# Kernel tuning notes

Hardware: AMD Instinct MI355X
Metric: run time of the kernel (lower is better)

Reference implementation:

```python
import jax, jax.numpy as jnp
import numpy as np

B, N, C = 8, 4096, 64          # graphs, points per graph, feature dim
RATIO = 0.25
M = int(N * RATIO)             # 1024 sampled centroids per graph
R = 0.2                        # radius (points live in the unit cube)
K = 64                         # max_num_neighbors in the forward
BIG = 1e10


def fps_single(pos):
    """Farthest point sampling on one cloud. pos: [N,3] -> [M] local indices.
    Deterministic start at index 0 (PyG uses a random start; math is identical)."""
    n = pos.shape[0]

    def step(carry, _):
        mind, last = carry
        d = jnp.sum((pos - pos[last]) ** 2, axis=-1)      # [N]
        mind = jnp.minimum(mind, d)
        nxt = jnp.argmax(mind)
        return (mind, nxt), nxt

    init = (jnp.full((n,), BIG, pos.dtype), jnp.int32(0))
    _, rest = jax.lax.scan(step, init, None, length=M - 1)
    return jnp.concatenate([jnp.zeros((1,), rest.dtype), rest])


def setup_inputs() -> dict:
    key = jax.random.key(0)
    ks = jax.random.split(key, 8)
    x = jax.random.normal(ks[0], (B * N, C), dtype=jnp.float32)
    pos = jax.random.uniform(ks[1], (B * N, 3), dtype=jnp.float32)
    batch = jnp.repeat(jnp.arange(B, dtype=jnp.int64), N)
    seed_idx = jnp.arange(B * N, dtype=jnp.int64)
    d_in, h, f_out = C + 3, 128, 256
    W1 = jax.random.normal(ks[2], (d_in, h), dtype=jnp.float32) / np.sqrt(d_in)
    b1 = jnp.zeros((h,), jnp.float32)
    W2 = jax.random.normal(ks[3], (h, h), dtype=jnp.float32) / np.sqrt(h)
    b2 = jnp.zeros((h,), jnp.float32)
    W3 = jax.random.normal(ks[4], (h, f_out), dtype=jnp.float32) / np.sqrt(h)
    b3 = jnp.zeros((f_out,), jnp.float32)
    return {"x": x, "pos": pos, "batch": batch, "seed_idx": seed_idx,
            "W1": W1, "b1": b1, "W2": W2, "b2": b2, "W3": W3, "b3": b3}


def reference(x, pos, batch, seed_idx, W1, b1, W2, b2, W3, b3):
    posb = pos.reshape(B, N, 3)
    xb = x.reshape(B, N, C)

    # --- FPS per graph (batch is block-contiguous with N points per graph) ---
    idx_local = jax.vmap(fps_single)(posb)                     # [B, M]
    ctr = jax.vmap(lambda p, i: p[i])(posb, idx_local)         # [B, M, 3]

    # --- radius neighbor search: up to K neighbors within r of each centroid ---
    d2 = jnp.sum((ctr[:, :, None, :] - posb[:, None, :, :]) ** 2, axis=-1)  # [B,M,N]
    d2m = jnp.where(d2 < R * R, d2, BIG)
    neg_d, nbr = jax.lax.top_k(-d2m, K)                        # K nearest within r
    valid = (-neg_d) < R * R                                   # [B, M, K]

    # --- PointConv: msg = MLP([x_j, pos_j - pos_i]), max-aggregate ---
    x_j = jax.vmap(lambda a, i: a[i])(xb, nbr)                 # [B, M, K, C]
    pos_j = jax.vmap(lambda p, i: p[i])(posb, nbr)             # [B, M, K, 3]
    msg = jnp.concatenate([x_j, pos_j - ctr[:, :, None, :]], axis=-1)  # [B,M,K,C+3]
    h = jax.nn.relu(msg @ W1 + b1)
    h = jax.nn.relu(h @ W2 + b2)
    h = jax.nn.relu(h @ W3 + b3)                               # [B, M, K, 256]
    h = jnp.where(valid[..., None], h, -BIG)
    out = jnp.max(h, axis=2)                                   # [B, M, 256]
    out = jnp.where(jnp.any(valid, axis=-1)[..., None], out, 0.0)

    # --- gather sampled outputs back to the flat layout ---
    idx_flat = (idx_local + jnp.arange(B)[:, None] * N).reshape(-1)  # [B*M]
    x_out = out.reshape(B * M, -1)
    pos_out = pos[idx_flat]
    batch_out = batch[idx_flat]
    seed_out = seed_idx[idx_flat]
    return x_out, pos_out, batch_out, seed_out
```

## Files before the change

kernel.cpp:

```cpp
#include <hip/hip_runtime.h>
#include <stdint.h>

#define BB 8
#define NN 4096
#define CC 64
#define MM 1024
#define EE (BB*MM)
#define KK 64
#define F3 256
#define SM 104
#define SH 136
#define CAP 768

typedef __bf16 bf16x8 __attribute__((ext_vector_type(8)));
typedef float floatx4 __attribute__((ext_vector_type(4)));

#define DPP_MAXSTEP(ctrl, rmask) { \
    unsigned o = (unsigned)__builtin_amdgcn_update_dpp(0, (int)v, ctrl, rmask, 0xf, false); \
    v = v > o ? v : o; }
__device__ __forceinline__ unsigned wave_umax_u32(unsigned v) {
  DPP_MAXSTEP(0x111, 0xf)
  DPP_MAXSTEP(0x112, 0xf)
  DPP_MAXSTEP(0x114, 0xf)
  DPP_MAXSTEP(0x118, 0xf)
  DPP_MAXSTEP(0x142, 0xa)
  DPP_MAXSTEP(0x143, 0xc)
  return (unsigned)__builtin_amdgcn_readlane((int)v, 63);
}
#define DPP_MINSTEP(ctrl, rmask) { \
    unsigned o = (unsigned)__builtin_amdgcn_update_dpp((int)0xffffffffu, (int)v, ctrl, rmask, 0xf, false); \
    v = v < o ? v : o; }
__device__ __forceinline__ unsigned wave_umin_u32(unsigned v) {
  DPP_MINSTEP(0x111, 0xf)
  DPP_MINSTEP(0x112, 0xf)
  DPP_MINSTEP(0x114, 0xf)
  DPP_MINSTEP(0x118, 0xf)
  DPP_MINSTEP(0x142, 0xa)
  DPP_MINSTEP(0x143, 0xc)
  return (unsigned)__builtin_amdgcn_readlane((int)v, 63);
}


__global__ __launch_bounds__(512) void fused_kernel(
    const float* __restrict__ x, const float* __restrict__ pos,
    const float* __restrict__ W1, const float* __restrict__ b1,
    const float* __restrict__ W2, const float* __restrict__ b2,
    const float* __restrict__ W3, const float* __restrict__ b3,
    int* __restrict__ fpsIdx, float* __restrict__ ctr,
    __bf16* __restrict__ W1t, __bf16* __restrict__ W2t, __bf16* __restrict__ W3t,
    float4* __restrict__ pos4, unsigned* __restrict__ ctl,
    float* __restrict__ outX, float* __restrict__ outP,
    float* __restrict__ outB, float* __restrict__ outS) {
  __shared__ __align__(16) unsigned char sBuf[65600];
  __shared__ unsigned sRole;

  const int t = threadIdx.x;

  if (t == 0)
    sRole = __hip_atomic_fetch_add(&ctl[288], 1u, __ATOMIC_RELAXED, __HIP_MEMORY_SCOPE_AGENT);
  __syncthreads();
  const unsigned role = sRole;

  if (role < BB) {
    const int g = (int)role;
    float4* sP4 = (float4*)sBuf;
    unsigned long long* sRed = (unsigned long long*)(sBuf + 65536);

    for (int k = g * 11776 + t; k < (g + 1) * 11776; k += 512) {
      if (k < 12288) {
        const int n = k / 96, kk = k % 96;
        W1t[k] = (kk < 67) ? (__bf16)W1[kk * 128 + n] : (__bf16)0.0f;
      } else if (k < 28672) {
        const int i = k - 12288, n = i / 128, kk = i % 128;
        W2t[i] = (__bf16)W2[kk * 128 + n];
      } else if (k < 61440) {
        const int i = k - 28672, n = i / 128, kk = i % 128;
        W3t[i] = (__bf16)W3[kk * 256 + n];
      } else {
        const int i = k - 61440;
        pos4[i] = make_float4(pos[(long)i * 3 + 0], pos[(long)i * 3 + 1],
                              pos[(long)i * 3 + 2], 0.0f);
      }
    }
    __threadfence();
    __syncthreads();
    if (t == 0)
      __hip_atomic_fetch_add(&ctl[0], 1u, __ATOMIC_RELEASE, __HIP_MEMORY_SCOPE_AGENT);

    __builtin_amdgcn_s_setprio(1);

    const int lane = t & 63, wv = t >> 6;
    float px[16], py[16], pz[16], mind[16];
    if (t < 256) {
#pragma unroll
      for (int j = 0; j < 16; ++j) {
        const int p = t + (j << 8);
        const long base = ((long)g * NN + p) * 3;
        px[j] = pos[base + 0];
        py[j] = pos[base + 1];
        pz[j] = pos[base + 2];
        mind[j] = 1e10f;
        sP4[p] = make_float4(px[j], py[j], pz[j], 0.0f);
      }
    }
    __syncthreads();
    float wx = 0.f, wy = 0.f, wz = 0.f;
    if (t < 256) { const float4 w0 = sP4[0]; wx = w0.x; wy = w0.y; wz = w0.z; }
    if (t == 0) {
      const long e0 = (long)g * MM;
      ctr[e0 * 3 + 0] = px[0]; ctr[e0 * 3 + 1] = py[0]; ctr[e0 * 3 + 2] = pz[0];
      fpsIdx[e0] = 0;
    }
    for (int s = 1; s < MM; ++s) {
      if (t < 256) {
        unsigned bb = 0u, bidx = (unsigned)t;
#pragma unroll
        for (int j = 0; j < 16; ++j) {
          const float dx = __fsub_rn(px[j], wx);
          const float dy = __fsub_rn(py[j], wy);
          const float dz = __fsub_rn(pz[j], wz);
          const float d2 = __fadd_rn(__fadd_rn(__fmul_rn(dx, dx), __fmul_rn(dy, dy)), __fmul_rn(dz, dz));
          mind[j] = fminf(mind[j], d2);
          const unsigned mb = __float_as_uint(mind[j]);
          if (mb > bb) { bb = mb; bidx = (unsigned)(t + (j << 8)); }
        }
        const unsigned maxv = wave_umax_u32(bb);
        const unsigned cand = (bb == maxv) ? bidx : 0xffffffffu;
        const unsigned widx_w = wave_umin_u32(cand);
        if (lane == 0)
          sRed[(s & 1) * 4 + wv] = ((unsigned long long)maxv << 32) | (unsigned long long)(~widx_w);
      }
      __syncthreads();
      if (t < 256) {
        unsigned long long m = sRed[(s & 1) * 4 + 0];
#pragma unroll
        for (int w = 1; w < 4; ++w) {
          const unsigned long long o = sRed[(s & 1) * 4 + w];
          m = o > m ? o : m;
        }
        const int widx = (int)(~(unsigned)m);
        const float4 wp = sP4[widx];
        wx = wp.x; wy = wp.y; wz = wp.z;
        if (t == 0) {
          const long eo = (long)g * MM + s;
          ctr[eo * 3 + 0] = wp.x; ctr[eo * 3 + 1] = wp.y; ctr[eo * 3 + 2] = wp.z;
          fpsIdx[eo] = widx;
          if ((s & 31) == 31)
            __hip_atomic_store(&ctl[32 * (g + 1)], (unsigned)(s + 1),
                               __ATOMIC_RELEASE, __HIP_MEMORY_SCOPE_AGENT);
        }
      }
    }
    return;
  }

  {
    const int item = (int)role - BB;
    if (item >= EE) return;
    const int g = item & 7, sidx = item >> 3;
    const int e = g * MM + sidx;
    const int b = g;

    __bf16* sMsg = (__bf16*)sBuf;
    __bf16* sH   = (__bf16*)(sBuf + 13312);
    int* sSel    = (int*)(sBuf + 30720);
    int* sCnt    = (int*)(sBuf + 30976);
    unsigned long long* sDI = (unsigned long long*)sBuf;

    if (t == 0) {
      while (__hip_atomic_load(&ctl[0], __ATOMIC_ACQUIRE, __HIP_MEMORY_SCOPE_AGENT) < (unsigned)BB)
        __builtin_amdgcn_s_sleep(8);
      while (__hip_atomic_load(&ctl[32 * (g + 1)], __ATOMIC_ACQUIRE, __HIP_MEMORY_SCOPE_AGENT)
             <= (unsigned)sidx)
        __builtin_amdgcn_s_sleep(8);
      *sCnt = 0;
    }
    __syncthreads();

    const int lane = t & 63, wv = t >> 6;
    const float cx = ctr[(long)e * 3 + 0];
    const float cy = ctr[(long)e * 3 + 1];
    const float cz = ctr[(long)e * 3 + 2];
    if (t < 3) outP[(long)e * 3 + t] = ctr[(long)e * 3 + t];
    if (t == 3) { outB[e] = (float)b; outS[e] = (float)(b * NN + fpsIdx[e]); }
    const float R2 = (float)(0.2 * 0.2);

#pragma unroll
    for (int q = 0; q < NN / 512; ++q) {
      const int p = t + q * 512;
      const float4 P = pos4[b * NN + p];
      const float dx = __fsub_rn(cx, P.x);
      const float dy = __fsub_rn(cy, P.y);
      const float dz = __fsub_rn(cz, P.z);
      const float d2 = __fadd_rn(__fadd_rn(__fmul_rn(dx, dx), __fmul_rn(dy, dy)), __fmul_rn(dz, dz));
      const bool v = d2 < R2;
      const unsigned long long mask = __ballot(v);
      int wbase = 0;
      if (lane == 0 && mask) wbase = atomicAdd(sCnt, (int)__popcll(mask));
      wbase = __shfl(wbase, 0);
      if (v) {
        const int off = wbase + (int)__popcll(mask & ((1ull << lane) - 1ull));
        if (off < CAP)
          sDI[off] = ((unsigned long long)__float_as_uint(d2) << 32) | (unsigned)p;
      }
    }
    __syncthreads();
    int cnt = *sCnt; cnt = cnt > CAP ? CAP : cnt;
    const int nsel = cnt < KK ? cnt : KK;

    for (int i = t; i < cnt; i += 512) {
      const unsigned long long my = sDI[i];
      int rank = 0;
#pragma unroll 8
      for (int j = 0; j < cnt; ++j) rank += (sDI[j] < my) ? 1 : 0;
      if (rank < KK) sSel[rank] = (int)(unsigned)(my & 0xffffffffu);
    }
    __syncthreads();
    cnt = nsel;

    {
      const int r = t >> 3, p = t & 7;
      float4 a = make_float4(0.f, 0.f, 0.f, 0.f), c4 = a;
      if (r < cnt) {
        const float* xr = x + (long)(b * NN + sSel[r]) * CC + p * 8;
        a  = *(const float4*)xr;
        c4 = *(const float4*)(xr + 4);
      }
      __bf16 o[8] = {(__bf16)a.x, (__bf16)a.y, (__bf16)a.z, (__bf16)a.w,
                     (__bf16)c4.x, (__bf16)c4.y, (__bf16)c4.z, (__bf16)c4.w};
      *(uint4*)&sMsg[r * SM + p * 8] = *(uint4*)o;
    }
    if (t < 64) {
      const int r = t;
      __bf16 d0 = (__bf16)0.0f, d1 = (__bf16)0.0f, d2v = (__bf16)0.0f;
      if (r < cnt) {
        const float4 P = pos4[b * NN + sSel[r]];
        d0  = (__bf16)__fsub_rn(P.x, cx);
        d1  = (__bf16)__fsub_rn(P.y, cy);
        d2v = (__bf16)__fsub_rn(P.z, cz);
      }
      sMsg[r * SM + 64] = d0;
      sMsg[r * SM + 65] = d1;
      sMsg[r * SM + 66] = d2v;
      for (int c = 67; c < SM; ++c) sMsg[r * SM + c] = (__bf16)0.0f;
    }
    __syncthreads();

    const int l15 = lane & 15, quad = lane >> 4;
    {
      floatx4 acc[4] = {};
      const __bf16* wrow = W1t + (wv * 16 + l15) * 96;
#pragma unroll
      for (int ks = 0; ks < 3; ++ks) {
        const bf16x8 bfrag = *(const bf16x8*)(wrow + ks * 32 + quad * 8);
#pragma unroll
        for (int mt = 0; mt < 4; ++mt) {
          const bf16x8 afrag = *(const bf16x8*)&sMsg[(mt * 16 + l15) * SM + ks * 32 + quad * 8];
          acc[mt] = __builtin_amdgcn_mfma_f32_16x16x32_bf16(afrag, bfrag, acc[mt], 0, 0, 0);
        }
      }
      const int col = wv * 16 + l15;
      const float bias = b1[col];
#pragma unroll
      for (int mt = 0; mt < 4; ++mt)
#pragma unroll
        for (int rg = 0; rg < 4; ++rg) {
          const int row = mt * 16 + quad * 4 + rg;
          float v = acc[mt][rg] + bias;
          v = v > 0.0f ? v : 0.0f;
          sH[row * SH + col] = (__bf16)v;
        }
    }
    __syncthreads();
    {
      floatx4 acc[4] = {};
      const __bf16* wrow = W2t + (wv * 16 + l15) * 128;
#pragma unroll
      for (int ks = 0; ks < 4; ++ks) {
        const bf16x8 bfrag = *(const bf16x8*)(wrow + ks * 32 + quad * 8);
#pragma unroll
        for (int mt = 0; mt < 4; ++mt) {
          const bf16x8 afrag = *(const bf16x8*)&sH[(mt * 16 + l15) * SH + ks * 32 + quad * 8];
          acc[mt] = __builtin_amdgcn_mfma_f32_16x16x32_bf16(afrag, bfrag, acc[mt], 0, 0, 0);
        }
      }
      __syncthreads();
      const int col = wv * 16 + l15;
      const float bias = b2[col];
#pragma unroll
      for (int mt = 0; mt < 4; ++mt)
#pragma unroll
        for (int rg = 0; rg < 4; ++rg) {
          const int row = mt * 16 + quad * 4 + rg;
          float v = acc[mt][rg] + bias;
          v = v > 0.0f ? v : 0.0f;
          sH[row * SH + col] = (__bf16)v;
        }
    }
    __syncthreads();
    {
      floatx4 acc[2][4] = {};
#pragma unroll
      for (int ks = 0; ks < 4; ++ks) {
        bf16x8 afrag[4];
#pragma unroll
        for (int mt = 0; mt < 4; ++mt)
          afrag[mt] = *(const bf16x8*)&sH[(mt * 16 + l15) * SH + ks * 32 + quad * 8];
#pragma unroll
        for (int i = 0; i < 2; ++i) {
          const bf16x8 bfrag = *(const bf16x8*)(W3t + ((wv * 2 + i) * 16 + l15) * 128 + ks * 32 + quad * 8);
#pragma unroll
          for (int mt = 0; mt < 4; ++mt)
            acc[i][mt] = __builtin_amdgcn_mfma_f32_16x16x32_bf16(afrag[mt], bfrag, acc[i][mt], 0, 0, 0);
        }
      }
#pragma unroll
      for (int i = 0; i < 2; ++i) {
        const int col = (wv * 2 + i) * 16 + l15;
        const float bias = b3[col];
        float mx = 0.0f;
#pragma unroll
        for (int mt = 0; mt < 4; ++mt)
#pragma unroll
          for (int rg = 0; rg < 4; ++rg) {
            const int row = mt * 16 + quad * 4 + rg;
            float v = acc[i][mt][rg] + bias;
            v = v > 0.0f ? v : 0.0f;
            if (row < cnt) mx = fmaxf(mx, v);
          }
        mx = fmaxf(mx, __shfl_xor(mx, 16));
        mx = fmaxf(mx, __shfl_xor(mx, 32));
        if (quad == 0) outX[(long)e * F3 + col] = mx;
      }
    }
  }
}

extern "C" void kernel_launch(void* const* d_in, const int* in_sizes, int n_in,
                              void* d_out, int out_size, void* d_ws, size_t ws_size,
                              hipStream_t stream) {
  const float* x   = (const float*)d_in[0];
  const float* pos = (const float*)d_in[1];
  const float* W1  = (const float*)d_in[4];
  const float* b1  = (const float*)d_in[5];
  const float* W2  = (const float*)d_in[6];
  const float* b2  = (const float*)d_in[7];
  const float* W3  = (const float*)d_in[8];
  const float* b3  = (const float*)d_in[9];

  char* ws = (char*)d_ws;
  int*    fpsIdx = (int*)(ws);
  float*  ctr    = (float*)(ws + 32768);
  __bf16* W1t    = (__bf16*)(ws + 131072);
  __bf16* W2t    = (__bf16*)(ws + 155648);
  __bf16* W3t    = (__bf16*)(ws + 188416);
  float4* pos4   = (float4*)(ws + 253952);
  unsigned* ctl  = (unsigned*)(ws + 778240);

  float* outX = (float*)d_out;
  float* outP = outX + (long)EE * F3;
  float* outB = outP + (long)EE * 3;
  float* outS = outB + EE;

  hipMemsetAsync(ctl, 0, 1280, stream);
  fused_kernel<<<BB + EE, 512, 0, stream>>>(x, pos, W1, b1, W2, b2, W3, b3,
                                            fpsIdx, ctr, W1t, W2t, W3t, pos4, ctl,
                                            outX, outP, outB, outS);
}
```

Before: 904.8 us.

## Use persistent work-queue blocks overlapping FPS plus a drain kernel; pack FPS math

```diff
diff --git a/kernel.cpp b/kernel.cpp
--- a/kernel.cpp
+++ b/kernel.cpp
@@ -14,6 +14,7 @@
 
 typedef __bf16 bf16x8 __attribute__((ext_vector_type(8)));
 typedef float floatx4 __attribute__((ext_vector_type(4)));
+typedef float f32x2 __attribute__((ext_vector_type(2)));
 
 #define DPP_MAXSTEP(ctrl, rmask) { \
     unsigned o = (unsigned)__builtin_amdgcn_update_dpp(0, (int)v, ctrl, rmask, 0xf, false); \
@@ -40,8 +41,183 @@
   return (unsigned)__builtin_amdgcn_readlane((int)v, 63);
 }
 
-
-__global__ __launch_bounds__(512) void fused_kernel(
+__device__ __forceinline__ void mlp_item(
+    int e, int b, int t,
+    const float* __restrict__ x, const float4* __restrict__ pos4,
+    const float* __restrict__ ctr, const int* __restrict__ fpsIdx,
+    const __bf16* __restrict__ W1t, const __bf16* __restrict__ W2t,
+    const __bf16* __restrict__ W3t,
+    const float* __restrict__ b1, const float* __restrict__ b2,
+    const float* __restrict__ b3,
+    float* __restrict__ outX, float* __restrict__ outP,
+    float* __restrict__ outB, float* __restrict__ outS,
+    __bf16* sMsg, __bf16* sH, int* sSel, int* sCnt) {
+  unsigned long long* sDI = (unsigned long long*)sMsg;
+  const int lane = t & 63, wv = t >> 6;
+
+  const float cx = ctr[(long)e * 3 + 0];
+  const float cy = ctr[(long)e * 3 + 1];
+  const float cz = ctr[(long)e * 3 + 2];
+  if (t < 3) outP[(long)e * 3 + t] = ctr[(long)e * 3 + t];
+  if (t == 3) { outB[e] = (float)b; outS[e] = (float)(b * NN + fpsIdx[e]); }
+  const float R2 = (float)(0.2 * 0.2);
+
+#pragma unroll
+  for (int q = 0; q < NN / 512; ++q) {
+    const int p = t + q * 512;
+    const float4 P = pos4[b * NN + p];
+    const float dx = __fsub_rn(cx, P.x);
+    const float dy = __fsub_rn(cy, P.y);
+    const float dz = __fsub_rn(cz, P.z);
+    const float d2 = __fadd_rn(__fadd_rn(__fmul_rn(dx, dx), __fmul_rn(dy, dy)), __fmul_rn(dz, dz));
+    const bool v = d2 < R2;
+    const unsigned long long mask = __ballot(v);
+    int wbase = 0;
+    if (lane == 0 && mask) wbase = atomicAdd(sCnt, (int)__popcll(mask));
+    wbase = __shfl(wbase, 0);
+    if (v) {
+      const int off = wbase + (int)__popcll(mask & ((1ull << lane) - 1ull));
+      if (off < CAP)
+        sDI[off] = ((unsigned long long)__float_as_uint(d2) << 32) | (unsigned)p;
+    }
+  }
+  __syncthreads();
+  int cnt = *sCnt; cnt = cnt > CAP ? CAP : cnt;
+  const int nsel = cnt < KK ? cnt : KK;
+
+  for (int i = t; i < cnt; i += 512) {
+    const unsigned long long my = sDI[i];
+    int rank = 0;
+#pragma unroll 8
+    for (int j = 0; j < cnt; ++j) rank += (sDI[j] < my) ? 1 : 0;
+    if (rank < KK) sSel[rank] = (int)(unsigned)(my & 0xffffffffu);
+  }
+  __syncthreads();
+  cnt = nsel;
+
+  {
+    const int r = t >> 3, p = t & 7;
+    float4 a = make_float4(0.f, 0.f, 0.f, 0.f), c4 = a;
+    if (r < cnt) {
+      const float* xr = x + (long)(b * NN + sSel[r]) * CC + p * 8;
+      a  = *(const float4*)xr;
+      c4 = *(const float4*)(xr + 4);
+    }
+    __bf16 o[8] = {(__bf16)a.x, (__bf16)a.y, (__bf16)a.z, (__bf16)a.w,
+                   (__bf16)c4.x, (__bf16)c4.y, (__bf16)c4.z, (__bf16)c4.w};
+    *(uint4*)&sMsg[r * SM + p * 8] = *(uint4*)o;
+  }
+  if (t < 64) {
+    const int r = t;
+    __bf16 d0 = (__bf16)0.0f, d1 = (__bf16)0.0f, d2v = (__bf16)0.0f;
+    if (r < cnt) {
+      const float4 P = pos4[b * NN + sSel[r]];
+      d0  = (__bf16)__fsub_rn(P.x, cx);
+      d1  = (__bf16)__fsub_rn(P.y, cy);
+      d2v = (__bf16)__fsub_rn(P.z, cz);
+    }
+    sMsg[r * SM + 64] = d0;
+    sMsg[r * SM + 65] = d1;
+    sMsg[r * SM + 66] = d2v;
+    for (int c = 67; c < SM; ++c) sMsg[r * SM + c] = (__bf16)0.0f;
+  }
+  __syncthreads();
+
+  const int l15 = lane & 15, quad = lane >> 4;
+  {
+    floatx4 acc[4] = {};
+    const __bf16* wrow = W1t + (wv * 16 + l15) * 96;
+#pragma unroll
+    for (int ks = 0; ks < 3; ++ks) {
+      const bf16x8 bfrag = *(const bf16x8*)(wrow + ks * 32 + quad * 8);
+#pragma unroll
+      for (int mt = 0; mt < 4; ++mt) {
+        const bf16x8 afrag = *(const bf16x8*)&sMsg[(mt * 16 + l15) * SM + ks * 32 + quad * 8];
+        acc[mt] = __builtin_amdgcn_mfma_f32_16x16x32_bf16(afrag, bfrag, acc[mt], 0, 0, 0);
+      }
+    }
+    const int col = wv * 16 + l15;
+    const float bias = b1[col];
+#pragma unroll
+    for (int mt = 0; mt < 4; ++mt)
+#pragma unroll
+      for (int rg = 0; rg < 4; ++rg) {
+        const int row = mt * 16 + quad * 4 + rg;
+        float v = acc[mt][rg] + bias;
+        v = v > 0.0f ? v : 0.0f;
+        sH[row * SH + col] = (__bf16)v;
+      }
+  }
+  __syncthreads();
+  {
+    floatx4 acc[4] = {};
+    const __bf16* wrow = W2t + (wv * 16 + l15) * 128;
+#pragma unroll
+    for (int ks = 0; ks < 4; ++ks) {
+      const bf16x8 bfrag = *(const bf16x8*)(wrow + ks * 32 + quad * 8);
+#pragma unroll
+      for (int mt = 0; mt < 4; ++mt) {
+        const bf16x8 afrag = *(const bf16x8*)&sH[(mt * 16 + l15) * SH + ks * 32 + quad * 8];
+        acc[mt] = __builtin_amdgcn_mfma_f32_16x16x32_bf16(afrag, bfrag, acc[mt], 0, 0, 0);
+      }
+    }
+    __syncthreads();
+    const int col = wv * 16 + l15;
+    const float bias = b2[col];
+#pragma unroll
+    for (int mt = 0; mt < 4; ++mt)
+#pragma unroll
+      for (int rg = 0; rg < 4; ++rg) {
+        const int row = mt * 16 + quad * 4 + rg;
+        float v = acc[mt][rg] + bias;
+        v = v > 0.0f ? v : 0.0f;
+        sH[row * SH + col] = (__bf16)v;
+      }
+  }
+  __syncthreads();
+  {
+    floatx4 acc[2][4] = {};
+#pragma unroll
+    for (int ks = 0; ks < 4; ++ks) {
+      bf16x8 afrag[4];
+#pragma unroll
+      for (int mt = 0; mt < 4; ++mt)
+        afrag[mt] = *(const bf16x8*)&sH[(mt * 16 + l15) * SH + ks * 32 + quad * 8];
+#pragma unroll
+      for (int i = 0; i < 2; ++i) {
+        const bf16x8 bfrag = *(const bf16x8*)(W3t + ((wv * 2 + i) * 16 + l15) * 128 + ks * 32 + quad * 8);
+#pragma unroll
+        for (int mt = 0; mt < 4; ++mt)
+          acc[i][mt] = __builtin_amdgcn_mfma_f32_16x16x32_bf16(afrag[mt], bfrag, acc[i][mt], 0, 0, 0);
+      }
+    }
+#pragma unroll
+    for (int i = 0; i < 2; ++i) {
+      const int col = (wv * 2 + i) * 16 + l15;
+      const float bias = b3[col];
+      float mx = 0.0f;
+#pragma unroll
+      for (int mt = 0; mt < 4; ++mt)
+#pragma unroll
+        for (int rg = 0; rg < 4; ++rg) {
+          const int row = mt * 16 + quad * 4 + rg;
+          float v = acc[i][mt][rg] + bias;
+          v = v > 0.0f ? v : 0.0f;
+          if (row < cnt) mx = fmaxf(mx, v);
+        }
+      mx = fmaxf(mx, __shfl_xor(mx, 16));
+      mx = fmaxf(mx, __shfl_xor(mx, 32));
+      if (quad == 0) outX[(long)e * F3 + col] = mx;
+    }
+  }
+}
+
+#define CTL_PREP 0
+#define CTL_PROG(g) (32*((g)+1))
+#define CTL_QHEAD 320
+#define CTL_DONE 352
+
+__global__ __launch_bounds__(512) void fps_overlap_kernel(
     const float* __restrict__ x, const float* __restrict__ pos,
     const float* __restrict__ W1, const float* __restrict__ b1,
     const float* __restrict__ W2, const float* __restrict__ b2,
@@ -52,17 +228,13 @@
     float* __restrict__ outX, float* __restrict__ outP,
     float* __restrict__ outB, float* __restrict__ outS) {
   __shared__ __align__(16) unsigned char sBuf[65600];
-  __shared__ unsigned sRole;
+  __shared__ int sClaim;
 
   const int t = threadIdx.x;
-
-  if (t == 0)
-    sRole = __hip_atomic_fetch_add(&ctl[288], 1u, __ATOMIC_RELAXED, __HIP_MEMORY_SCOPE_AGENT);
-  __syncthreads();
-  const unsigned role = sRole;
-
-  if (role < BB) {
-    const int g = (int)role;
+  const int blk = blockIdx.x;
+
+  if (blk < BB) {
+    const int g = blk;
     float4* sP4 = (float4*)sBuf;
     unsigned long long* sRed = (unsigned long long*)(sBuf + 65536);
 
@@ -85,22 +257,24 @@
     __threadfence();
     __syncthreads();
     if (t == 0)
-      __hip_atomic_fetch_add(&ctl[0], 1u, __ATOMIC_RELEASE, __HIP_MEMORY_SCOPE_AGENT);
+      __hip_atomic_fetch_add(&ctl[CTL_PREP], 1u, __ATOMIC_RELEASE, __HIP_MEMORY_SCOPE_AGENT);
 
     __builtin_amdgcn_s_setprio(1);
 
     const int lane = t & 63, wv = t >> 6;
-    float px[16], py[16], pz[16], mind[16];
+    f32x2 px2[8], py2[8], pz2[8], mind2[8];
     if (t < 256) {
 #pragma unroll
       for (int j = 0; j < 16; ++j) {
         const int p = t + (j << 8);
         const long base = ((long)g * NN + p) * 3;
-        px[j] = pos[base + 0];
-        py[j] = pos[base + 1];
-        pz[j] = pos[base + 2];
-        mind[j] = 1e10f;
-        sP4[p] = make_float4(px[j], py[j], pz[j], 0.0f);
+        const float X = pos[base + 0], Y = pos[base + 1], Z = pos[base + 2];
+        if ((j & 1) == 0) {
+          px2[j >> 1].x = X; py2[j >> 1].x = Y; pz2[j >> 1].x = Z; mind2[j >> 1].x = 1e10f;
+        } else {
+          px2[j >> 1].y = X; py2[j >> 1].y = Y; pz2[j >> 1].y = Z; mind2[j >> 1].y = 1e10f;
+        }
+        sP4[p] = make_float4(X, Y, Z, 0.0f);
       }
     }
     __syncthreads();
@@ -108,21 +282,42 @@
     if (t < 256) { const float4 w0 = sP4[0]; wx = w0.x; wy = w0.y; wz = w0.z; }
     if (t == 0) {
       const long e0 = (long)g * MM;
-      ctr[e0 * 3 + 0] = px[0]; ctr[e0 * 3 + 1] = py[0]; ctr[e0 * 3 + 2] = pz[0];
+      ctr[e0 * 3 + 0] = wx; ctr[e0 * 3 + 1] = wy; ctr[e0 * 3 + 2] = wz;
       fpsIdx[e0] = 0;
     }
     for (int s = 1; s < MM; ++s) {
       if (t < 256) {
-        unsigned bb = 0u, bidx = (unsigned)t;
-#pragma unroll
-        for (int j = 0; j < 16; ++j) {
-          const float dx = __fsub_rn(px[j], wx);
-          const float dy = __fsub_rn(py[j], wy);
-          const float dz = __fsub_rn(pz[j], wz);
-          const float d2 = __fadd_rn(__fadd_rn(__fmul_rn(dx, dx), __fmul_rn(dy, dy)), __fmul_rn(dz, dz));
-          mind[j] = fminf(mind[j], d2);
-          const unsigned mb = __float_as_uint(mind[j]);
-          if (mb > bb) { bb = mb; bidx = (unsigned)(t + (j << 8)); }
+        unsigned bb, bidx;
+        {
+#pragma clang fp contract(off)
+          float tv[8]; int tj[8];
+#pragma unroll
+          for (int k = 0; k < 8; ++k) {
+            f32x2 dx = px2[k] - wx;
+            f32x2 dy = py2[k] - wy;
+            f32x2 dz = pz2[k] - wz;
+            f32x2 xx = dx * dx;
+            f32x2 yy = dy * dy;
+            f32x2 zz = dz * dz;
+            f32x2 s2 = xx + yy;
+            f32x2 d2 = s2 + zz;
+            mind2[k] = __builtin_elementwise_min(mind2[k], d2);
+            const float a = mind2[k].x, bq = mind2[k].y;
+            const bool gt = bq > a;
+            tv[k] = gt ? bq : a;
+            tj[k] = gt ? (k * 2 + 1) : (k * 2);
+          }
+#pragma unroll
+          for (int st = 0; st < 3; ++st) {
+#pragma unroll
+            for (int i = 0; i < (4 >> st); ++i) {
+              const bool gt = tv[2 * i + 1] > tv[2 * i];
+              tv[i] = gt ? tv[2 * i + 1] : tv[2 * i];
+              tj[i] = gt ? tj[2 * i + 1] : tj[2 * i];
+            }
+          }
+          bb = __float_as_uint(tv[0]);
+          bidx = (unsigned)t + ((unsigned)tj[0] << 8);
         }
         const unsigned maxv = wave_umax_u32(bb);
         const unsigned cand = (bb == maxv) ? bidx : 0xffffffffu;
@@ -146,194 +341,83 @@
           ctr[eo * 3 + 0] = wp.x; ctr[eo * 3 + 1] = wp.y; ctr[eo * 3 + 2] = wp.z;
           fpsIdx[eo] = widx;
           if ((s & 31) == 31)
-            __hip_atomic_store(&ctl[32 * (g + 1)], (unsigned)(s + 1),
+            __hip_atomic_store(&ctl[CTL_PROG(g)], (unsigned)(s + 1),
                                __ATOMIC_RELEASE, __HIP_MEMORY_SCOPE_AGENT);
         }
       }
     }
+    if (t == 0)
+      __hip_atomic_fetch_add(&ctl[CTL_DONE], 1u, __ATOMIC_RELEASE, __HIP_MEMORY_SCOPE_AGENT);
     return;
   }
 
   {
-    const int item = (int)role - BB;
-    if (item >= EE) return;
-    const int g = item & 7, sidx = item >> 3;
-    const int e = g * MM + sidx;
-    const int b = g;
-
     __bf16* sMsg = (__bf16*)sBuf;
     __bf16* sH   = (__bf16*)(sBuf + 13312);
     int* sSel    = (int*)(sBuf + 30720);
     int* sCnt    = (int*)(sBuf + 30976);
-    unsigned long long* sDI = (unsigned long long*)sBuf;
 
     if (t == 0) {
-      while (__hip_atomic_load(&ctl[0], __ATOMIC_ACQUIRE, __HIP_MEMORY_SCOPE_AGENT) < (unsigned)BB)
+      while (__hip_atomic_load(&ctl[CTL_PREP], __ATOMIC_ACQUIRE, __HIP_MEMORY_SCOPE_AGENT) < (unsigned)BB)
         __builtin_amdgcn_s_sleep(8);
-      while (__hip_atomic_load(&ctl[32 * (g + 1)], __ATOMIC_ACQUIRE, __HIP_MEMORY_SCOPE_AGENT)
-             <= (unsigned)sidx)
-        __builtin_amdgcn_s_sleep(8);
-      *sCnt = 0;
     }
     __syncthreads();
 
-    const int lane = t & 63, wv = t >> 6;
-    const float cx = ctr[(long)e * 3 + 0];
-    const float cy = ctr[(long)e * 3 + 1];
-    const float cz = ctr[(long)e * 3 + 2];
-    if (t < 3) outP[(long)e * 3 + t] = ctr[(long)e * 3 + t];
-    if (t == 3) { outB[e] = (float)b; outS[e] = (float)(b * NN + fpsIdx[e]); }
-    const float R2 = (float)(0.2 * 0.2);
-
-#pragma unroll
-    for (int q = 0; q < NN / 512; ++q) {
-      const int p = t + q * 512;
-      const float4 P = pos4[b * NN + p];
-      const float dx = __fsub_rn(cx, P.x);
-      const float dy = __fsub_rn(cy, P.y);
-      const float dz = __fsub_rn(cz, P.z);
-      const float d2 = __fadd_rn(__fadd_rn(__fmul_rn(dx, dx), __fmul_rn(dy, dy)), __fmul_rn(dz, dz));
-      const bool v = d2 < R2;
-      const unsigned long long mask = __ballot(v);
-      int wbase = 0;
-      if (lane == 0 && mask) wbase = atomicAdd(sCnt, (int)__popcll(mask));
-      wbase = __shfl(wbase, 0);
-      if (v) {
-        const int off = wbase + (int)__popcll(mask & ((1ull << lane) - 1ull));
-        if (off < CAP)
-          sDI[off] = ((unsigned long long)__float_as_uint(d2) << 32) | (unsigned)p;
-      }
-    }
-    __syncthreads();
-    int cnt = *sCnt; cnt = cnt > CAP ? CAP : cnt;
-    const int nsel = cnt < KK ? cnt : KK;
-
-    for (int i = t; i < cnt; i += 512) {
-      const unsigned long long my = sDI[i];
-      int rank = 0;
-#pragma unroll 8
-      for (int j = 0; j < cnt; ++j) rank += (sDI[j] < my) ? 1 : 0;
-      if (rank < KK) sSel[rank] = (int)(unsigned)(my & 0xffffffffu);
-    }
-    __syncthreads();
-    cnt = nsel;
-
-    {
-      const int r = t >> 3, p = t & 7;
-      float4 a = make_float4(0.f, 0.f, 0.f, 0.f), c4 = a;
-      if (r < cnt) {
-        const float* xr = x + (long)(b * NN + sSel[r]) * CC + p * 8;
-        a  = *(const float4*)xr;
-        c4 = *(const float4*)(xr + 4);
-      }
-      __bf16 o[8] = {(__bf16)a.x, (__bf16)a.y, (__bf16)a.z, (__bf16)a.w,
-                     (__bf16)c4.x, (__bf16)c4.y, (__bf16)c4.z, (__bf16)c4.w};
-      *(uint4*)&sMsg[r * SM + p * 8] = *(uint4*)o;
-    }
-    if (t < 64) {
-      const int r = t;
-      __bf16 d0 = (__bf16)0.0f, d1 = (__bf16)0.0f, d2v = (__bf16)0.0f;
-      if (r < cnt) {
-        const float4 P = pos4[b * NN + sSel[r]];
-        d0  = (__bf16)__fsub_rn(P.x, cx);
-        d1  = (__bf16)__fsub_rn(P.y, cy);
-        d2v = (__bf16)__fsub_rn(P.z, cz);
-      }
-      sMsg[r * SM + 64] = d0;
-      sMsg[r * SM + 65] = d1;
-      sMsg[r * SM + 66] = d2v;
-      for (int c = 67; c < SM; ++c) sMsg[r * SM + c] = (__bf16)0.0f;
-    }
-    __syncthreads();
-
-    const int l15 = lane & 15, quad = lane >> 4;
-    {
-      floatx4 acc[4] = {};
-      const __bf16* wrow = W1t + (wv * 16 + l15) * 96;
-#pragma unroll
-      for (int ks = 0; ks < 3; ++ks) {
-        const bf16x8 bfrag = *(const bf16x8*)(wrow + ks * 32 + quad * 8);
-#pragma unroll
-        for (int mt = 0; mt < 4; ++mt) {
-          const bf16x8 afrag = *(const bf16x8*)&sMsg[(mt * 16 + l15) * SM + ks * 32 + quad * 8];
-          acc[mt] = __builtin_amdgcn_mfma_f32_16x16x32_bf16(afrag, bfrag, acc[mt], 0, 0, 0);
-        }
-      }
-      const int col = wv * 16 + l15;
-      const float bias = b1[col];
-#pragma unroll
-      for (int mt = 0; mt < 4; ++mt)
-#pragma unroll
-        for (int rg = 0; rg < 4; ++rg) {
-          const int row = mt * 16 + quad * 4 + rg;
-          float v = acc[mt][rg] + bias;
-          v = v > 0.0f ? v : 0.0f;
-          sH[row * SH + col] = (__bf16)v;
-        }
-    }
-    __syncthreads();
-    {
-      floatx4 acc[4] = {};
-      const __bf16* wrow = W2t + (wv * 16 + l15) * 128;
-#pragma unroll
-      for (int ks = 0; ks < 4; ++ks) {
-        const bf16x8 bfrag = *(const bf16x8*)(wrow + ks * 32 + quad * 8);
-#pragma unroll
-        for (int mt = 0; mt < 4; ++mt) {
-          const bf16x8 afrag = *(const bf16x8*)&sH[(mt * 16 + l15) * SH + ks * 32 + quad * 8];
-          acc[mt] = __builtin_amdgcn_mfma_f32_16x16x32_bf16(afrag, bfrag, acc[mt], 0, 0, 0);
-        }
+    for (;;) {
+      if (t == 0) {
+        unsigned c;
+        const unsigned dn = __hip_atomic_load(&ctl[CTL_DONE], __ATOMIC_ACQUIRE, __HIP_MEMORY_SCOPE_AGENT);
+        if (dn >= (unsigned)BB) c = EE;
+        else c = __hip_atomic_fetch_add(&ctl[CTL_QHEAD], 1u, __ATOMIC_RELAXED, __HIP_MEMORY_SCOPE_AGENT);
+        sClaim = (int)c;
       }
       __syncthreads();
-      const int col = wv * 16 + l15;
-      const float bias = b2[col];
-#pragma unroll
-      for (int mt = 0; mt < 4; ++mt)
-#pragma unroll
-        for (int rg = 0; rg < 4; ++rg) {
-          const int row = mt * 16 + quad * 4 + rg;
-          float v = acc[mt][rg] + bias;
-          v = v > 0.0f ? v : 0.0f;
-          sH[row * SH + col] = (__bf16)v;
-        }
-    }
-    __syncthreads();
-    {
-      floatx4 acc[2][4] = {};
-#pragma unroll
-      for (int ks = 0; ks < 4; ++ks) {
-        bf16x8 afrag[4];
-#pragma unroll
-        for (int mt = 0; mt < 4; ++mt)
-          afrag[mt] = *(const bf16x8*)&sH[(mt * 16 + l15) * SH + ks * 32 + quad * 8];
-#pragma unroll
-        for (int i = 0; i < 2; ++i) {
-          const bf16x8 bfrag = *(const bf16x8*)(W3t + ((wv * 2 + i) * 16 + l15) * 128 + ks * 32 + quad * 8);
-#pragma unroll
-          for (int mt = 0; mt < 4; ++mt)
-            acc[i][mt] = __builtin_amdgcn_mfma_f32_16x16x32_bf16(afrag[mt], bfrag, acc[i][mt], 0, 0, 0);
-        }
-      }
-#pragma unroll
-      for (int i = 0; i < 2; ++i) {
-        const int col = (wv * 2 + i) * 16 + l15;
-        const float bias = b3[col];
-        float mx = 0.0f;
-#pragma unroll
-        for (int mt = 0; mt < 4; ++mt)
-#pragma unroll
-          for (int rg = 0; rg < 4; ++rg) {
-            const int row = mt * 16 + quad * 4 + rg;
-            float v = acc[i][mt][rg] + bias;
-            v = v > 0.0f ? v : 0.0f;
-            if (row < cnt) mx = fmaxf(mx, v);
-          }
-        mx = fmaxf(mx, __shfl_xor(mx, 16));
-        mx = fmaxf(mx, __shfl_xor(mx, 32));
-        if (quad == 0) outX[(long)e * F3 + col] = mx;
-      }
-    }
-  }
+      const int c = sClaim;
+      if (c >= EE) return;
+      const int g = c & 7, sidx = c >> 3;
+      const int e = g * MM + sidx;
+      if (t == 0) {
+        while (__hip_atomic_load(&ctl[CTL_PROG(g)], __ATOMIC_ACQUIRE, __HIP_MEMORY_SCOPE_AGENT)
+               <= (unsigned)sidx)
+          __builtin_amdgcn_s_sleep(8);
+        *sCnt = 0;
+      }
+      __syncthreads();
+      mlp_item(e, g, t, x, pos4, ctr, fpsIdx, W1t, W2t, W3t, b1, b2, b3,
+               outX, outP, outB, outS, sMsg, sH, sSel, sCnt);
+    }
+  }
+}
+
+__global__ __launch_bounds__(512) void drain_kernel(
+    const float* __restrict__ x, const float4* __restrict__ pos4,
+    const float* __restrict__ ctr, const int* __restrict__ fpsIdx,
+    const __bf16* __restrict__ W1t, const __bf16* __restrict__ W2t,
+    const __bf16* __restrict__ W3t,
+    const float* __restrict__ b1, const float* __restrict__ b2,
+    const float* __restrict__ b3, unsigned* __restrict__ ctl,
+    float* __restrict__ outX, float* __restrict__ outP,
+    float* __restrict__ outB, float* __restrict__ outS) {
+  __shared__ __align__(16) __bf16 sMsg[64 * SM];
+  __shared__ __align__(16) __bf16 sH[64 * SH];
+  __shared__ int sSel[KK];
+  __shared__ int sCnt;
+  __shared__ int sClaim;
+  const int t = threadIdx.x;
+
+  if (t == 0) {
+    unsigned c = __hip_atomic_load(&ctl[CTL_QHEAD], __ATOMIC_RELAXED, __HIP_MEMORY_SCOPE_AGENT);
+    if (c < (unsigned)EE)
+      c = __hip_atomic_fetch_add(&ctl[CTL_QHEAD], 1u, __ATOMIC_RELAXED, __HIP_MEMORY_SCOPE_AGENT);
+    sClaim = (int)c;
+    sCnt = 0;
+  }
+  __syncthreads();
+  const int c = sClaim;
+  if (c >= EE) return;
+  const int g = c & 7, sidx = c >> 3;
+  mlp_item(g * MM + sidx, g, t, x, pos4, ctr, fpsIdx, W1t, W2t, W3t, b1, b2, b3,
+           outX, outP, outB, outS, sMsg, sH, sSel, &sCnt);
 }
 
 extern "C" void kernel_launch(void* const* d_in, const int* in_sizes, int n_in,
@@ -362,8 +446,10 @@
   float* outB = outP + (long)EE * 3;
   float* outS = outB + EE;
 
-  hipMemsetAsync(ctl, 0, 1280, stream);
-  fused_kernel<<<BB + EE, 512, 0, stream>>>(x, pos, W1, b1, W2, b2, W3, b3,
-                                            fpsIdx, ctr, W1t, W2t, W3t, pos4, ctl,
-                                            outX, outP, outB, outS);
-}
+  hipMemsetAsync(ctl, 0, 2048, stream);
+  fps_overlap_kernel<<<256, 512, 0, stream>>>(x, pos, W1, b1, W2, b2, W3, b3,
+                                              fpsIdx, ctr, W1t, W2t, W3t, pos4, ctl,
+                                              outX, outP, outB, outS);
+  drain_kernel<<<EE, 512, 0, stream>>>(x, pos4, ctr, fpsIdx, W1t, W2t, W3t,
+                                       b1, b2, b3, ctl, outX, outP, outB, outS);
+}
```

Result: slower. 949.5 us (+4.9%).
